# Kernel tuning notes

Measured on AMD Instinct MI355X. Metric: run time of the kernel, lower is better.

## Reference

```python
import jax, jax.numpy as jnp
import numpy as np

B, Q, P = 8, 300, 5
RS, QS, CS, NC = 256, 768, 768, 396
HW = [64, 32, 16, 8]
POOL = [32, 16, 8, 4]
THR = 0.2


def _ln(x, g, b, eps=1e-5):
    m = x.mean(-1, keepdims=True)
    v = ((x - m) ** 2).mean(-1, keepdims=True)
    return (x - m) / jnp.sqrt(v + eps) * g + b


def _avgpool(x, oh, ow):
    # exact adaptive avg pool (output divides input)
    b, c, h, w = x.shape
    return x.reshape(b, c, oh, h // oh, ow, w // ow).mean((3, 5))


def setup_inputs() -> dict:
    key = jax.random.key(0)
    ks = jax.random.split(key, 40)
    inp = {}
    inp['pred_logits'] = jax.random.normal(ks[0], (B, Q, P), dtype=jnp.float32)
    inp['pred_boxes'] = jax.random.uniform(ks[1], (B, Q, 4), dtype=jnp.float32)
    inp['hs'] = jax.random.normal(ks[2], (B, Q, RS), dtype=jnp.float32)
    for s in range(4):
        inp[f'feat{s}'] = jax.random.normal(ks[3 + s], (B, 256, HW[s], HW[s]), dtype=jnp.float32)
        inp[f'pos{s}'] = jax.random.normal(ks[7 + s], (B, 256, HW[s], HW[s]), dtype=jnp.float32)
        inp[f'mask{s}'] = jax.random.bernoulli(ks[11 + s], 0.15, (B, HW[s], HW[s]))
        inp[f'convW{s}'] = jax.random.normal(ks[15 + s], (CS, 256), dtype=jnp.float32) * 0.02
        inp[f'convb{s}'] = jnp.zeros((CS,), jnp.float32)
        inp[f'lng{s}'] = jnp.ones((CS,), jnp.float32)
        inp[f'lnb{s}'] = jnp.zeros((CS,), jnp.float32)
    inp['learnable_query'] = jax.random.normal(ks[19], (P + 1, QS), dtype=jnp.float32)
    inp['Wq'] = jax.random.normal(ks[20], (RS, QS), dtype=jnp.float32) * 0.02
    inp['bq'] = jnp.zeros((QS,), jnp.float32)
    inp['qng'] = jnp.ones((QS,), jnp.float32)
    inp['qnb'] = jnp.zeros((QS,), jnp.float32)
    inp['W1'] = jax.random.normal(ks[21], (QS, QS), dtype=jnp.float32) * 0.02
    inp['b1'] = jnp.zeros((QS,), jnp.float32)
    inp['W2'] = jax.random.normal(ks[22], (QS, NC), dtype=jnp.float32) * 0.02
    inp['b2'] = jnp.zeros((NC,), jnp.float32)
    return inp


def _forward(pred_logits, pred_boxes, hs,
             feats, poss, masks, convWs, convbs, lngs, lnbs,
             learnable_query, Wq, bq, qng, qnb, W1, b1, W2, b2):
    del pred_boxes  # selected in the original but never used
    b = hs.shape[0]
    prob = jax.nn.sigmoid(pred_logits)                       # (B,Q,P)
    # per-prompt membership: logit_i > thr (implies max > thr)
    m = (prob > THR).astype(hs.dtype)                        # (B,Q,P)
    cnt = m.sum(1)                                           # (B,P)
    ssum = jnp.einsum('bqp,bqd->bpd', m, hs)                 # segment-sum over queries
    pooled = jnp.where(cnt[..., None] > 0,
                       ssum / jnp.maximum(cnt, 1.0)[..., None], 0.0)  # (B,P,RS)
    proj = pooled @ Wq + bq                                  # (B,P,QS)
    any_sel = jnp.any(prob.max(-1) > THR, axis=1)            # (B,)
    # if no query passed the global gate, prompt_hs is zeros WITHOUT projection
    prompt_hs = jnp.where(any_sel[:, None, None], proj, 0.0)
    prompt_query = learnable_query[1:] + prompt_hs           # (B,P,QS)
    cls_query = jnp.broadcast_to(learnable_query[0][None, None, :], (b, 1, QS))
    query_tokens = jnp.concatenate([cls_query, prompt_query], axis=1)
    query_tokens = _ln(query_tokens, qng, qnb)               # (B,P+1,QS)

    tokens = []
    for s in range(4):
        mask_f = masks[s][:, None, :, :].astype(feats[s].dtype)   # (B,1,H,W)
        x = (feats[s] + poss[s]) * (1.0 - mask_f)                 # masked_fill
        ctx = jnp.einsum('bchw,oc->bohw', x, convWs[s]) + convbs[s][None, :, None, None]
        p = _avgpool(ctx, POOL[s], POOL[s])
        mp = jnp.clip(_avgpool(1.0 - mask_f, POOL[s], POOL[s]), 1e-6, None)
        p = p / mp
        t = p.reshape(b, CS, -1).transpose(0, 2, 1)               # (B,T_s,CS)
        tokens.append(_ln(t, lngs[s], lnbs[s]))
    ctx_all = jnp.concatenate(tokens, axis=1)                     # (B,1360,CS)

    # encoder stand-in: fuse context into query tokens additively
    last = query_tokens + ctx_all.mean(1)[:, None, :]
    cls_logit = last[:, 0]
    prompt_logit = last[:, 1:].mean(1)
    h = jax.nn.relu((cls_logit + prompt_logit) @ W1 + b1)
    return h @ W2 + b2                                            # (B,NC)


def reference(pred_logits, pred_boxes, hs,
              feat0, pos0, mask0, convW0, convb0, lng0, lnb0,
              feat1, pos1, mask1, convW1, convb1, lng1, lnb1,
              feat2, pos2, mask2, convW2, convb2, lng2, lnb2,
              feat3, pos3, mask3, convW3, convb3, lng3, lnb3,
              learnable_query, Wq, bq, qng, qnb, W1, b1, W2, b2):
    return _forward(pred_logits, pred_boxes, hs,
                    [feat0, feat1, feat2, feat3],
                    [pos0, pos1, pos2, pos3],
                    [mask0, mask1, mask2, mask3],
                    [convW0, convW1, convW2, convW3],
                    [convb0, convb1, convb2, convb3],
                    [lng0, lng1, lng2, lng3],
                    [lnb0, lnb1, lnb2, lnb3],
                    learnable_query, Wq, bq, qng, qnb, W1, b1, W2, b2)
```

## Files before the change

### kernel.cpp

```cpp
#include <hip/hip_runtime.h>
#include <hip/hip_bf16.h>

#define Bn 8
#define Qn 300
#define Pn 5
#define RSn 256
#define QSn 768
#define NCn 396
#define MTOT 10880
#define THRL -1.3862943611198906f

typedef __attribute__((ext_vector_type(8))) short short8;
typedef __attribute__((ext_vector_type(4))) float float4v;

__device__ inline float wred(float v){
  #pragma unroll
  for (int off = 32; off; off >>= 1) v += __shfl_xor(v, off);
  return v;
}

__device__ __forceinline__ unsigned short f2bf(float f){
  union { float f; unsigned int u; } c; c.f = f;
  return (unsigned short)((c.u + 0x7FFF + ((c.u >> 16) & 1)) >> 16);
}

__global__ __launch_bounds__(256, 4) void k_front(
    const float* cw0, const float* cw1, const float* cw2, const float* cw3,
    short* Wswz, const int* __restrict__ mk0, int* det,
    const float* __restrict__ pl, const float* __restrict__ hs,
    float* pooled, int* flags, float* ctxsum, float* outz){
  int bx = blockIdx.x;
  int t = threadIdx.x;
  if (bx < 768){
    int s = bx / 192;
    int linear = (bx % 192)*256 + t;
    int q = linear & 63, n = linear >> 6;
    const float* src = (s==0)?cw0:(s==1)?cw1:(s==2)?cw2:cw3;
    float4 f = *(const float4*)(src + (size_t)n*256 + q*4);
    int kc = q >> 3, lk = (q >> 1) & 3, e0 = (q & 1)*4;
    short* dst = Wswz + ((size_t)(s*8 + kc))*24576 + lk*6144 + n*8 + e0;
    short4 sv;
    sv.x = (short)f2bf(f.x); sv.y = (short)f2bf(f.y);
    sv.z = (short)f2bf(f.z); sv.w = (short)f2bf(f.w);
    *(short4*)dst = sv;
    return;
  }
  if (bx == 768){
    __shared__ int r0[4], r1[4];
    const int* mm = mk0 + t*32;
    int d0 = 0, d1 = 0;
    #pragma unroll 8
    for (int i = 0; i < 32; ++i){
      int v = mm[i];
      d0 |= (v != 0 && v != 1);
      d1 |= (v != 0 && v != 0x3F800000);
    }
    unsigned long long bal0 = __ballot(d0), bal1 = __ballot(d1);
    int wid = t >> 6;
    if ((t & 63) == 0){ r0[wid] = (bal0 != 0ull); r1[wid] = (bal1 != 0ull); }
    __syncthreads();
    if (t == 0){
      det[0] = r0[0] | r0[1] | r0[2] | r0[3];
      det[1] = r1[0] | r1[1] | r1[2] | r1[3];
    }
    return;
  }
  if (bx >= 821){
    int idx = ((bx - 821)*256 + t)*4;
    if (idx < Bn*NCn) *(float4*)(outz + idx) = (float4){0.f,0.f,0.f,0.f};
    return;
  }
  if (bx >= 809){
    int idx = ((bx - 809)*256 + t)*4;
    *(float4*)(ctxsum + idx) = (float4){0.f,0.f,0.f,0.f};
    return;
  }
  __shared__ float msk[Qn];
  int bb = (bx - 769) / Pn, p = (bx - 769) % Pn;
  for (int q = t; q < Qn; q += 256)
    msk[q] = (pl[(bb*Qn + q)*Pn + p] > THRL) ? 1.f : 0.f;
  __syncthreads();
  const float* hb = hs + (size_t)bb*Qn*RSn + t;
  float s0 = 0.f, s1 = 0.f, s2 = 0.f, s3 = 0.f, cnt = 0.f;
  for (int q = 0; q < Qn; q += 4){
    float m0v = msk[q], m1 = msk[q+1], m2 = msk[q+2], m3 = msk[q+3];
    cnt += m0v + m1 + m2 + m3;
    s0 = fmaf(m0v, hb[(size_t)(q  )*RSn], s0);
    s1 = fmaf(m1,  hb[(size_t)(q+1)*RSn], s1);
    s2 = fmaf(m2,  hb[(size_t)(q+2)*RSn], s2);
    s3 = fmaf(m3,  hb[(size_t)(q+3)*RSn], s3);
  }
  float ssum = (s0 + s1) + (s2 + s3);
  pooled[(bb*Pn + p)*RSn + t] = (cnt > 0.f) ? ssum / cnt : 0.f;
  if (t == 0) flags[bb*Pn + p] = (cnt > 0.f) ? 1 : 0;
}

__global__ __launch_bounds__(256, 3) void k_pgemm(
    const float* fe0, const float* po0, const void* ma0,
    const float* fe1, const float* po1, const void* ma1,
    const float* fe2, const float* po2, const void* ma2,
    const float* fe3, const float* po3, const void* ma3,
    const int* __restrict__ det, const short* __restrict__ Wswz,
    const float* cb0, const float* cb1, const float* cb2, const float* cb3,
    const float* lg0, const float* lb0, const float* lg1, const float* lb1,
    const float* lg2, const float* lb2, const float* lg3, const float* lb3,
    float* __restrict__ ctxsum,
    const float* __restrict__ lq, const float* __restrict__ Wq,
    const float* __restrict__ bq, const float* __restrict__ qng,
    const float* __restrict__ qnb, const float* __restrict__ pooled,
    const int* __restrict__ flags, float* qt){
  __shared__ short As[16*264];
  __shared__ float wls[16][4];
  __shared__ float scls[16], imls[16];
  __shared__ float lsum[4][16], lsq[4][16];
  __shared__ float pq[256];
  __shared__ float s1s[4], s2s[4];
  int blk = blockIdx.x;
  int t = threadIdx.x;

  if (blk >= 680){
    int qbx = blk - 680;
    int b = qbx / 6, j = qbx % 6;
    float v0 = lq[j*QSn + t], v1 = lq[j*QSn + t + 256], v2 = lq[j*QSn + t + 512];
    int any = flags[b*Pn] | flags[b*Pn+1] | flags[b*Pn+2] | flags[b*Pn+3] | flags[b*Pn+4];
    if (j > 0 && any){
      pq[t] = pooled[(b*Pn + (j-1))*RSn + t];
      __syncthreads();
      float a0 = 0.f, a1 = 0.f, a2 = 0.f;
      #pragma unroll 8
      for (int c = 0; c < RSn; ++c){
        float pv = pq[c];
        a0 = fmaf(pv, Wq[c*QSn + t      ], a0);
        a1 = fmaf(pv, Wq[c*QSn + t + 256], a1);
        a2 = fmaf(pv, Wq[c*QSn + t + 512], a2);
      }
      v0 += a0 + bq[t]; v1 += a1 + bq[t+256]; v2 += a2 + bq[t+512];
    }
    float sm = v0 + v1 + v2, sq = v0*v0 + v1*v1 + v2*v2;
    sm = wred(sm); sq = wred(sq);
    int wid = t >> 6, lane = t & 63;
    if (lane == 0){ s1s[wid] = sm; s2s[wid] = sq; }
    __syncthreads();
    float S  = s1s[0] + s1s[1] + s1s[2] + s1s[3];
    float SQ = s2s[0] + s2s[1] + s2s[2] + s2s[3];
    float mu = S * (1.f/QSn), var = SQ * (1.f/QSn) - mu*mu;
    float rs = rsqrtf(var + 1e-5f);
    float* o = qt + (b*6 + j)*QSn;
    o[t      ] = (v0 - mu)*rs*qng[t      ] + qnb[t      ];
    o[t + 256] = (v1 - mu)*rs*qng[t + 256] + qnb[t + 256];
    o[t + 512] = (v2 - mu)*rs*qng[t + 512] + qnb[t + 512];
    return;
  }

  int m0 = blk * 16;
  int s, H, OWlog, b0;
  const float *F, *Pp; const void* M;
  const float *CB, *LG, *LB;
  if (m0 < 8192){ s=0; F=fe0; Pp=po0; M=ma0; H=64; OWlog=5; b0=m0>>10;
                  CB=cb0; LG=lg0; LB=lb0; }
  else if (m0 < 10240){ s=1; F=fe1; Pp=po1; M=ma1; H=32; OWlog=4; b0=(m0-8192)>>8;
                  CB=cb1; LG=lg1; LB=lb1; }
  else if (m0 < 10752){ s=2; F=fe2; Pp=po2; M=ma2; H=16; OWlog=3; b0=(m0-10240)>>6;
                  CB=cb2; LG=lg2; LB=lb2; }
  else { s=3; F=fe3; Pp=po3; M=ma3; H=8; OWlog=2; b0=(m0-10752)>>4;
                  CB=cb3; LG=lg3; LB=lb3; }
  int HH = H*H;
  int OWm = (H >> 1) - 1;
  int mode = (det[0] == 0) ? 0 : ((det[1] == 0) ? 2 : 1);

  int slot = t & 15;
  int gm = m0 + slot;
  int bb = b0;
  int ltl;
  if (s == 0)      ltl = gm & 1023;
  else if (s == 1) ltl = gm & 255;
  else if (s == 2) ltl = gm & 63;
  else             ltl = gm & 15;
  int ph = ltl >> OWlog, pw = ltl & OWm;
  int i00 = ph*2*H + pw*2;
  int mbase = bb*HH;

  if (t < 16){
    float w0, w1, w2, w3;
    if (mode == 0){
      const int* Mi = (const int*)M + mbase + i00;
      int2 ma = *(const int2*)(Mi);
      int2 mb = *(const int2*)(Mi + H);
      w0 = ma.x?0.f:1.f; w1 = ma.y?0.f:1.f; w2 = mb.x?0.f:1.f; w3 = mb.y?0.f:1.f;
    } else if (mode == 1){
      const unsigned char* Mb = (const unsigned char*)M + mbase + i00;
      w0 = Mb[0]?0.f:1.f; w1 = Mb[1]?0.f:1.f; w2 = Mb[H]?0.f:1.f; w3 = Mb[H+1]?0.f:1.f;
    } else {
      const float* Mf = (const float*)M + mbase + i00;
      float2 ma = *(const float2*)(Mf);
      float2 mb = *(const float2*)(Mf + H);
      w0 = 1.f-ma.x; w1 = 1.f-ma.y; w2 = 1.f-mb.x; w3 = 1.f-mb.y;
    }
    float msum = w0 + w1 + w2 + w3;
    float im = 1.f / fmaxf(msum*0.25f, 1e-6f);
    wls[t][0] = w0; wls[t][1] = w1; wls[t][2] = w2; wls[t][3] = w3;
    scls[t] = 0.25f*im; imls[t] = im;
  }
  __syncthreads();

  {
    float w0 = wls[slot][0], w1 = wls[slot][1], w2 = wls[slot][2], w3 = wls[slot][3];
    float sc = scls[slot];
    int chb = (t >> 4) * 2;
    size_t base = (size_t)(bb*256 + chb)*HH + i00;
    const float* Fp = F + base;
    const float* Pq = Pp + base;
    const int stride = 32*HH;
    #pragma unroll 2
    for (int r = 0; r < 8; ++r){
      float2 fa0 = *(const float2*)(Fp);
      float2 fb0 = *(const float2*)(Fp + H);
      float2 pa0 = *(const float2*)(Pq);
      float2 pb0 = *(const float2*)(Pq + H);
      float2 fa1 = *(const float2*)(Fp + HH);
      float2 fb1 = *(const float2*)(Fp + HH + H);
      float2 pa1 = *(const float2*)(Pq + HH);
      float2 pb1 = *(const float2*)(Pq + HH + H);
      float x0 = (fa0.x+pa0.x)*w0 + (fa0.y+pa0.y)*w1 + (fb0.x+pb0.x)*w2 + (fb0.y+pb0.y)*w3;
      float x1 = (fa1.x+pa1.x)*w0 + (fa1.y+pa1.y)*w1 + (fb1.x+pb1.x)*w2 + (fb1.y+pb1.y)*w3;
      *(unsigned int*)(&As[slot*264 + chb + r*32]) =
          (unsigned int)f2bf(x0*sc) | ((unsigned int)f2bf(x1*sc) << 16);
      Fp += stride; Pq += stride;
    }
  }
  __syncthreads();

  int wid = t >> 6, l = t & 63;
  int lm = l & 15, lk = l >> 4;
  int nfb = wid * 12;
  short8 aReg[8];
  #pragma unroll
  for (int kc = 0; kc < 8; ++kc)
    aReg[kc] = *(const short8*)(As + lm*264 + kc*32 + lk*8);

  float4v acc[12];
  #pragma unroll
  for (int nf = 0; nf < 12; ++nf) acc[nf] = (float4v){0.f,0.f,0.f,0.f};

  const short* Bb = Wswz + ((size_t)(s*8))*24576 + lk*6144 + nfb*128 + lm*8;
  #pragma unroll
  for (int kc = 0; kc < 8; ++kc){
    const short* bp = Bb + kc*24576;
    #pragma unroll
    for (int nf = 0; nf < 12; ++nf){
      short8 bf = *(const short8*)(bp + nf*128);
      acc[nf] = __builtin_amdgcn_mfma_f32_16x16x32_bf16(aReg[kc], bf, acc[nf], 0, 0, 0);
    }
  }

  float im4[4];
  #pragma unroll
  for (int r = 0; r < 4; ++r) im4[r] = imls[lk*4 + r];

  float sum[4] = {0,0,0,0}, sq[4] = {0,0,0,0};
  #pragma unroll
  for (int nf = 0; nf < 12; ++nf){
    float cbv = CB[(nfb+nf)*16 + lm];
    #pragma unroll
    for (int r = 0; r < 4; ++r){
      float p = acc[nf][r] + cbv*im4[r];
      acc[nf][r] = p;
      sum[r] += p;
      sq[r] = fmaf(p, p, sq[r]);
    }
  }
  #pragma unroll
  for (int r = 0; r < 4; ++r){
    #pragma unroll
    for (int off = 1; off < 16; off <<= 1){
      sum[r] += __shfl_xor(sum[r], off);
      sq[r]  += __shfl_xor(sq[r],  off);
    }
  }
  if (lm == 0){
    #pragma unroll
    for (int r = 0; r < 4; ++r){
      lsum[wid][lk*4 + r] = sum[r];
      lsq[wid][lk*4 + r]  = sq[r];
    }
  }
  __syncthreads();
  float mu[4], rs[4];
  #pragma unroll
  for (int r = 0; r < 4; ++r){
    int row = lk*4 + r;
    float S  = lsum[0][row] + lsum[1][row] + lsum[2][row] + lsum[3][row];
    float SQ = lsq[0][row]  + lsq[1][row]  + lsq[2][row]  + lsq[3][row];
    mu[r] = S * (1.f/768.f);
    float var = SQ * (1.f/768.f) - mu[r]*mu[r];
    rs[r] = rsqrtf(var + 1e-5f);
  }
  #pragma unroll
  for (int nf = 0; nf < 12; ++nf){
    int n = (nfb+nf)*16 + lm;
    float g = LG[n], bv = LB[n];
    float tv = 0.f;
    #pragma unroll
    for (int r = 0; r < 4; ++r)
      tv += (acc[nf][r] - mu[r]) * rs[r];
    tv = tv*g + 4.f*bv;
    tv += __shfl_xor(tv, 16); tv += __shfl_xor(tv, 32);
    if (lk == 0)
      atomicAdd(&ctxsum[b0*768 + n], tv);
  }
}

__global__ void k_hpre(const float* __restrict__ qt, const float* __restrict__ ctxsum,
                       const float* __restrict__ W1, const float* __restrict__ b1,
                       float* __restrict__ hpre){
  __shared__ float vsh[Bn][192];
  int nc = blockIdx.x % 24, kc = blockIdx.x / 24;
  int n0 = nc*32, c0 = kc*192;
  int t = threadIdx.x;
  for (int i = t; i < Bn*192; i += 256){
    int b = i / 192, cl = i - b*192;
    int c = c0 + cl;
    const float* q = qt + (size_t)b*6*768;
    float pm = q[768+c] + q[2*768+c] + q[3*768+c] + q[4*768+c] + q[5*768+c];
    vsh[b][cl] = q[c] + 0.2f*pm + ctxsum[b*768 + c]*(1.f/680.f);
  }
  __syncthreads();
  int ow = t & 31, bi = t >> 5;
  int o = n0 + ow;
  float acc = 0.f;
  const float* w = W1 + (size_t)c0*768 + o;
  #pragma unroll 4
  for (int cl = 0; cl < 192; ++cl)
    acc = fmaf(vsh[bi][cl], w[(size_t)cl*768], acc);
  if (kc == 0) acc += b1[o];
  atomicAdd(&hpre[bi*768 + o], acc);
}

__global__ void k_out(const float* __restrict__ hpre, const float* __restrict__ W2,
                      const float* __restrict__ b2, float* __restrict__ out){
  __shared__ float hsh[Bn][192];
  int nc = blockIdx.x % 13, kc = blockIdx.x / 13;
  int n0 = nc*32, c0 = kc*192;
  int t = threadIdx.x;
  for (int i = t; i < Bn*192; i += 256){
    int b = i / 192, cl = i - b*192;
    hsh[b][cl] = fmaxf(hpre[b*768 + c0 + cl], 0.f);
  }
  __syncthreads();
  int ow = t & 31, bi = t >> 5;
  int o = n0 + ow;
  if (o >= NCn) return;
  float acc = 0.f;
  const float* w = W2 + (size_t)c0*NCn + o;
  #pragma unroll 4
  for (int cl = 0; cl < 192; ++cl)
    acc = fmaf(hsh[bi][cl], w[(size_t)cl*NCn], acc);
  if (kc == 0) acc += b2[o];
  atomicAdd(&out[bi*NCn + o], acc);
}

extern "C" void kernel_launch(void* const* d_in, const int* in_sizes, int n_in,
                              void* d_out, int out_size, void* d_ws, size_t ws_size,
                              hipStream_t stream){
  const float* pl = (const float*)d_in[0];
  const float* hs = (const float*)d_in[2];
  const float* feat[4]; const float* pos[4]; const void* mask[4];
  const float* cw[4]; const float* cb[4]; const float* lg[4]; const float* lb[4];
  for (int s = 0; s < 4; ++s){
    int base = 3 + 7*s;
    feat[s] = (const float*)d_in[base];
    pos[s]  = (const float*)d_in[base+1];
    mask[s] = d_in[base+2];
    cw[s]   = (const float*)d_in[base+3];
    cb[s]   = (const float*)d_in[base+4];
    lg[s]   = (const float*)d_in[base+5];
    lb[s]   = (const float*)d_in[base+6];
  }
  const float* lq  = (const float*)d_in[31];
  const float* Wq  = (const float*)d_in[32];
  const float* bq  = (const float*)d_in[33];
  const float* qng = (const float*)d_in[34];
  const float* qnb = (const float*)d_in[35];
  const float* W1  = (const float*)d_in[36];
  const float* b1  = (const float*)d_in[37];
  const float* W2  = (const float*)d_in[38];
  const float* b2  = (const float*)d_in[39];
  float* out = (float*)d_out;

  short* Wswz   = (short*)d_ws;
  float* pooled = (float*)(Wswz + (size_t)4*8*4*768*8);
  float* qt     = pooled + 40*RSn;
  float* ctxsum = qt + Bn*6*QSn;
  float* hpre   = ctxsum + Bn*QSn;
  int*   det    = (int*)(hpre + Bn*QSn);
  int*   flags  = det + 4;

  k_front<<<825, 256, 0, stream>>>(cw[0], cw[1], cw[2], cw[3], Wswz,
                                   (const int*)mask[0], det, pl, hs, pooled, flags,
                                   ctxsum, out);
  k_pgemm<<<728, 256, 0, stream>>>(feat[0], pos[0], mask[0],
                                   feat[1], pos[1], mask[1],
                                   feat[2], pos[2], mask[2],
                                   feat[3], pos[3], mask[3],
                                   det, Wswz,
                                   cb[0], cb[1], cb[2], cb[3],
                                   lg[0], lb[0], lg[1], lb[1],
                                   lg[2], lb[2], lg[3], lb[3], ctxsum,
                                   lq, Wq, bq, qng, qnb, pooled, flags, qt);
  k_hpre<<<96, 256, 0, stream>>>(qt, ctxsum, W1, b1, hpre);
  k_out<<<52, 256, 0, stream>>>(hpre, W2, b2, out);
}
```

Measured before the change: 269.5 us.

## Split pooling into separate kernel and stage GEMM weights via direct-to-LDS loads

Pulls the masked 2x2 avg-pool of feat+pos out of the projection GEMM into its own kernel. That kernel uses wider float4 loads and writes a bf16 activation buffer plus per-row inverse-mask scales to workspace. The GEMM kernel then reads A rows from global memory and stages each 48KB weight K-slice into shared memory with global_load_lds, replacing per-lane global reads of B. This adds a kernel launch, an extra global round trip for the activations, and two barriers per K step, and it lowers occupancy because of the large shared buffer.

New measurement: 284.9 us. 1.06x slower.

```diff
diff --git a/kernel.cpp b/kernel.cpp
--- a/kernel.cpp
+++ b/kernel.cpp
@@ -22,6 +22,12 @@
 __device__ __forceinline__ unsigned short f2bf(float f){
   union { float f; unsigned int u; } c; c.f = f;
   return (unsigned short)((c.u + 0x7FFF + ((c.u >> 16) & 1)) >> 16);
+}
+
+__device__ __forceinline__ void gld_lds16(const short* g, short* l){
+  __builtin_amdgcn_global_load_lds(
+      (const __attribute__((address_space(1))) void*)g,
+      (__attribute__((address_space(3))) void*)l, 16, 0, 0);
 }
 
 __global__ __launch_bounds__(256, 4) void k_front(
@@ -95,12 +101,87 @@
   if (t == 0) flags[bb*Pn + p] = (cnt > 0.f) ? 1 : 0;
 }
 
-__global__ __launch_bounds__(256, 3) void k_pgemm(
+__global__ __launch_bounds__(512, 2) void k_pool(
     const float* fe0, const float* po0, const void* ma0,
     const float* fe1, const float* po1, const void* ma1,
     const float* fe2, const float* po2, const void* ma2,
     const float* fe3, const float* po3, const void* ma3,
-    const int* __restrict__ det, const short* __restrict__ Wswz,
+    const int* __restrict__ det,
+    short* __restrict__ Abuf, float* __restrict__ imtab){
+  int blk = blockIdx.x;
+  int t = threadIdx.x;
+  int m0 = blk * 16;
+  int s, H, OWlog, b0;
+  const float *F, *Pp; const void* M;
+  if (m0 < 8192){ s=0; F=fe0; Pp=po0; M=ma0; H=64; OWlog=5; b0=m0>>10; }
+  else if (m0 < 10240){ s=1; F=fe1; Pp=po1; M=ma1; H=32; OWlog=4; b0=(m0-8192)>>8; }
+  else if (m0 < 10752){ s=2; F=fe2; Pp=po2; M=ma2; H=16; OWlog=3; b0=(m0-10240)>>6; }
+  else { s=3; F=fe3; Pp=po3; M=ma3; H=8; OWlog=2; b0=(m0-10752)>>4; }
+  int HH = H*H;
+  int OWm = (H >> 1) - 1;
+  int mode = (det[0] == 0) ? 0 : ((det[1] == 0) ? 2 : 1);
+
+  int slotp = t & 7;
+  int mA = m0 + slotp*2;
+  int ltl;
+  if (s == 0)      ltl = mA & 1023;
+  else if (s == 1) ltl = mA & 255;
+  else if (s == 2) ltl = mA & 63;
+  else             ltl = mA & 15;
+  int ph = ltl >> OWlog, pw = ltl & OWm;
+  int i00 = ph*2*H + pw*2;
+  int mbase = b0*HH;
+
+  float w0A,w1A,w2A,w3A, w0B,w1B,w2B,w3B;
+  if (mode == 0){
+    const int* Mi = (const int*)M + mbase + i00;
+    int4 ma = *(const int4*)(Mi);
+    int4 mb = *(const int4*)(Mi + H);
+    w0A = ma.x?0.f:1.f; w1A = ma.y?0.f:1.f; w2A = mb.x?0.f:1.f; w3A = mb.y?0.f:1.f;
+    w0B = ma.z?0.f:1.f; w1B = ma.w?0.f:1.f; w2B = mb.z?0.f:1.f; w3B = mb.w?0.f:1.f;
+  } else if (mode == 1){
+    const unsigned char* Mb = (const unsigned char*)M + mbase + i00;
+    uchar4 av = *(const uchar4*)(Mb);
+    uchar4 bv = *(const uchar4*)(Mb + H);
+    w0A = av.x?0.f:1.f; w1A = av.y?0.f:1.f; w2A = bv.x?0.f:1.f; w3A = bv.y?0.f:1.f;
+    w0B = av.z?0.f:1.f; w1B = av.w?0.f:1.f; w2B = bv.z?0.f:1.f; w3B = bv.w?0.f:1.f;
+  } else {
+    const float* Mf = (const float*)M + mbase + i00;
+    float4 ma = *(const float4*)(Mf);
+    float4 mb = *(const float4*)(Mf + H);
+    w0A = 1.f-ma.x; w1A = 1.f-ma.y; w2A = 1.f-mb.x; w3A = 1.f-mb.y;
+    w0B = 1.f-ma.z; w1B = 1.f-ma.w; w2B = 1.f-mb.z; w3B = 1.f-mb.w;
+  }
+  float msA = w0A+w1A+w2A+w3A, msB = w0B+w1B+w2B+w3B;
+  float imA = 1.f / fmaxf(msA*0.25f, 1e-6f);
+  float imB = 1.f / fmaxf(msB*0.25f, 1e-6f);
+  float scA = 0.25f*imA, scB = 0.25f*imB;
+  if ((t >> 3) == 0){ imtab[mA] = imA; imtab[mA+1] = imB; }
+
+  int cg = t >> 3;
+  size_t base = (size_t)(b0*256 + cg)*HH + i00;
+  const float* Fp = F + base;
+  const float* Pq = Pp + base;
+  short* oA = Abuf + (size_t)mA*256 + cg;
+  short* oB = oA + 256;
+  const size_t stride = (size_t)64*HH;
+  #pragma unroll
+  for (int r = 0; r < 4; ++r){
+    float4 f0 = *(const float4*)(Fp);
+    float4 f1 = *(const float4*)(Fp + H);
+    float4 p0 = *(const float4*)(Pq);
+    float4 p1 = *(const float4*)(Pq + H);
+    float xA = (f0.x+p0.x)*w0A + (f0.y+p0.y)*w1A + (f1.x+p1.x)*w2A + (f1.y+p1.y)*w3A;
+    float xB = (f0.z+p0.z)*w0B + (f0.w+p0.w)*w1B + (f1.z+p1.z)*w2B + (f1.w+p1.w)*w3B;
+    oA[r*64] = (short)f2bf(xA*scA);
+    oB[r*64] = (short)f2bf(xB*scB);
+    Fp += stride; Pq += stride;
+  }
+}
+
+__global__ __launch_bounds__(256, 2) void k_pgemm(
+    const short* __restrict__ Abuf, const float* __restrict__ imtab,
+    const short* __restrict__ Wswz,
     const float* cb0, const float* cb1, const float* cb2, const float* cb3,
     const float* lg0, const float* lb0, const float* lg1, const float* lb1,
     const float* lg2, const float* lb2, const float* lg3, const float* lb3,
@@ -109,9 +190,7 @@
     const float* __restrict__ bq, const float* __restrict__ qng,
     const float* __restrict__ qnb, const float* __restrict__ pooled,
     const int* __restrict__ flags, float* qt){
-  __shared__ short As[16*264];
-  __shared__ float wls[16][4];
-  __shared__ float scls[16], imls[16];
+  __shared__ short Bsh[24576];
   __shared__ float lsum[4][16], lsq[4][16];
   __shared__ float pq[256];
   __shared__ float s1s[4], s2s[4];
@@ -153,109 +232,47 @@
   }
 
   int m0 = blk * 16;
-  int s, H, OWlog, b0;
-  const float *F, *Pp; const void* M;
+  int s, b0;
   const float *CB, *LG, *LB;
-  if (m0 < 8192){ s=0; F=fe0; Pp=po0; M=ma0; H=64; OWlog=5; b0=m0>>10;
-                  CB=cb0; LG=lg0; LB=lb0; }
-  else if (m0 < 10240){ s=1; F=fe1; Pp=po1; M=ma1; H=32; OWlog=4; b0=(m0-8192)>>8;
-                  CB=cb1; LG=lg1; LB=lb1; }
-  else if (m0 < 10752){ s=2; F=fe2; Pp=po2; M=ma2; H=16; OWlog=3; b0=(m0-10240)>>6;
-                  CB=cb2; LG=lg2; LB=lb2; }
-  else { s=3; F=fe3; Pp=po3; M=ma3; H=8; OWlog=2; b0=(m0-10752)>>4;
-                  CB=cb3; LG=lg3; LB=lb3; }
-  int HH = H*H;
-  int OWm = (H >> 1) - 1;
-  int mode = (det[0] == 0) ? 0 : ((det[1] == 0) ? 2 : 1);
-
-  int slot = t & 15;
-  int gm = m0 + slot;
-  int bb = b0;
-  int ltl;
-  if (s == 0)      ltl = gm & 1023;
-  else if (s == 1) ltl = gm & 255;
-  else if (s == 2) ltl = gm & 63;
-  else             ltl = gm & 15;
-  int ph = ltl >> OWlog, pw = ltl & OWm;
-  int i00 = ph*2*H + pw*2;
-  int mbase = bb*HH;
-
-  if (t < 16){
-    float w0, w1, w2, w3;
-    if (mode == 0){
-      const int* Mi = (const int*)M + mbase + i00;
-      int2 ma = *(const int2*)(Mi);
-      int2 mb = *(const int2*)(Mi + H);
-      w0 = ma.x?0.f:1.f; w1 = ma.y?0.f:1.f; w2 = mb.x?0.f:1.f; w3 = mb.y?0.f:1.f;
-    } else if (mode == 1){
-      const unsigned char* Mb = (const unsigned char*)M + mbase + i00;
-      w0 = Mb[0]?0.f:1.f; w1 = Mb[1]?0.f:1.f; w2 = Mb[H]?0.f:1.f; w3 = Mb[H+1]?0.f:1.f;
-    } else {
-      const float* Mf = (const float*)M + mbase + i00;
-      float2 ma = *(const float2*)(Mf);
-      float2 mb = *(const float2*)(Mf + H);
-      w0 = 1.f-ma.x; w1 = 1.f-ma.y; w2 = 1.f-mb.x; w3 = 1.f-mb.y;
-    }
-    float msum = w0 + w1 + w2 + w3;
-    float im = 1.f / fmaxf(msum*0.25f, 1e-6f);
-    wls[t][0] = w0; wls[t][1] = w1; wls[t][2] = w2; wls[t][3] = w3;
-    scls[t] = 0.25f*im; imls[t] = im;
-  }
-  __syncthreads();
-
-  {
-    float w0 = wls[slot][0], w1 = wls[slot][1], w2 = wls[slot][2], w3 = wls[slot][3];
-    float sc = scls[slot];
-    int chb = (t >> 4) * 2;
-    size_t base = (size_t)(bb*256 + chb)*HH + i00;
-    const float* Fp = F + base;
-    const float* Pq = Pp + base;
-    const int stride = 32*HH;
-    #pragma unroll 2
-    for (int r = 0; r < 8; ++r){
-      float2 fa0 = *(const float2*)(Fp);
-      float2 fb0 = *(const float2*)(Fp + H);
-      float2 pa0 = *(const float2*)(Pq);
-      float2 pb0 = *(const float2*)(Pq + H);
-      float2 fa1 = *(const float2*)(Fp + HH);
-      float2 fb1 = *(const float2*)(Fp + HH + H);
-      float2 pa1 = *(const float2*)(Pq + HH);
-      float2 pb1 = *(const float2*)(Pq + HH + H);
-      float x0 = (fa0.x+pa0.x)*w0 + (fa0.y+pa0.y)*w1 + (fb0.x+pb0.x)*w2 + (fb0.y+pb0.y)*w3;
-      float x1 = (fa1.x+pa1.x)*w0 + (fa1.y+pa1.y)*w1 + (fb1.x+pb1.x)*w2 + (fb1.y+pb1.y)*w3;
-      *(unsigned int*)(&As[slot*264 + chb + r*32]) =
-          (unsigned int)f2bf(x0*sc) | ((unsigned int)f2bf(x1*sc) << 16);
-      Fp += stride; Pq += stride;
-    }
-  }
-  __syncthreads();
+  if (m0 < 8192){ s=0; b0=m0>>10; CB=cb0; LG=lg0; LB=lb0; }
+  else if (m0 < 10240){ s=1; b0=(m0-8192)>>8; CB=cb1; LG=lg1; LB=lb1; }
+  else if (m0 < 10752){ s=2; b0=(m0-10240)>>6; CB=cb2; LG=lg2; LB=lb2; }
+  else { s=3; b0=(m0-10752)>>4; CB=cb3; LG=lg3; LB=lb3; }
 
   int wid = t >> 6, l = t & 63;
   int lm = l & 15, lk = l >> 4;
   int nfb = wid * 12;
+
   short8 aReg[8];
   #pragma unroll
   for (int kc = 0; kc < 8; ++kc)
-    aReg[kc] = *(const short8*)(As + lm*264 + kc*32 + lk*8);
+    aReg[kc] = *(const short8*)(Abuf + (size_t)(m0 + lm)*256 + kc*32 + lk*8);
 
   float4v acc[12];
   #pragma unroll
   for (int nf = 0; nf < 12; ++nf) acc[nf] = (float4v){0.f,0.f,0.f,0.f};
 
-  const short* Bb = Wswz + ((size_t)(s*8))*24576 + lk*6144 + nfb*128 + lm*8;
   #pragma unroll
   for (int kc = 0; kc < 8; ++kc){
-    const short* bp = Bb + kc*24576;
+    const short* slice = Wswz + ((size_t)(s*8 + kc))*24576;
+    #pragma unroll
+    for (int j = 0; j < 12; ++j){
+      int chunk = wid*12 + j;
+      gld_lds16(slice + chunk*512 + l*8, Bsh + chunk*512);
+    }
+    __syncthreads();
+    const short* bb2 = Bsh + lk*6144 + lm*8;
     #pragma unroll
     for (int nf = 0; nf < 12; ++nf){
-      short8 bf = *(const short8*)(bp + nf*128);
+      short8 bf = *(const short8*)(bb2 + (size_t)(nfb+nf)*128);
       acc[nf] = __builtin_amdgcn_mfma_f32_16x16x32_bf16(aReg[kc], bf, acc[nf], 0, 0, 0);
     }
+    __syncthreads();
   }
 
   float im4[4];
   #pragma unroll
-  for (int r = 0; r < 4; ++r) im4[r] = imls[lk*4 + r];
+  for (int r = 0; r < 4; ++r) im4[r] = imtab[m0 + lk*4 + r];
 
   float sum[4] = {0,0,0,0}, sq[4] = {0,0,0,0};
   #pragma unroll
@@ -388,21 +405,24 @@
   float* out = (float*)d_out;
 
   short* Wswz   = (short*)d_ws;
-  float* pooled = (float*)(Wswz + (size_t)4*8*4*768*8);
+  short* Abuf   = Wswz + (size_t)4*8*4*768*8;
+  float* pooled = (float*)(Abuf + (size_t)MTOT*256);
   float* qt     = pooled + 40*RSn;
   float* ctxsum = qt + Bn*6*QSn;
   float* hpre   = ctxsum + Bn*QSn;
-  int*   det    = (int*)(hpre + Bn*QSn);
+  float* imtab  = hpre + Bn*QSn;
+  int*   det    = (int*)(imtab + MTOT);
   int*   flags  = det + 4;
 
   k_front<<<825, 256, 0, stream>>>(cw[0], cw[1], cw[2], cw[3], Wswz,
                                    (const int*)mask[0], det, pl, hs, pooled, flags,
                                    ctxsum, out);
-  k_pgemm<<<728, 256, 0, stream>>>(feat[0], pos[0], mask[0],
-                                   feat[1], pos[1], mask[1],
-                                   feat[2], pos[2], mask[2],
-                                   feat[3], pos[3], mask[3],
-                                   det, Wswz,
+  k_pool<<<680, 512, 0, stream>>>(feat[0], pos[0], mask[0],
+                                  feat[1], pos[1], mask[1],
+                                  feat[2], pos[2], mask[2],
+                                  feat[3], pos[3], mask[3],
+                                  det, Abuf, imtab);
+  k_pgemm<<<728, 256, 0, stream>>>(Abuf, imtab, Wswz,
                                    cb[0], cb[1], cb[2], cb[3],
                                    lg[0], lb[0], lg[1], lb[1],
                                    lg[2], lb[2], lg[3], lb[3], ctxsum,
```
